# Performance work log

Hardware: AMD Instinct MI355X
Metric: run time of the kernel (lower is better)

## Reference

```python
import jax, jax.numpy as jnp
import numpy as np

N_NODES = 200000
N_EDGES = 800000
N_GRAPHS = 4096
ATOM_DIM = 128
HIDDEN = 256
LN_EPS = 1e-5


def _layer_norm(x, g, b):
    m = jnp.mean(x, axis=-1, keepdims=True)
    v = jnp.mean((x - m) ** 2, axis=-1, keepdims=True)
    return (x - m) / jnp.sqrt(v + LN_EPS) * g + b


def setup_inputs() -> dict:
    key = jax.random.key(0)
    ks = jax.random.split(key, 16)
    d = {}
    d['x'] = jax.random.normal(ks[0], (N_NODES, ATOM_DIM), dtype=jnp.float32)
    d['edge_index'] = jax.random.randint(ks[1], (2, N_EDGES), 0, N_NODES, dtype=jnp.int32)
    # sorted batch assignment covering all graphs (PyG batches are sorted)
    d['batch'] = ((jnp.arange(N_NODES) * N_GRAPHS) // N_NODES).astype(jnp.int32)

    def glorot(k, shape):
        fan_in, fan_out = shape[0], shape[1]
        s = jnp.sqrt(2.0 / (fan_in + fan_out))
        return jax.random.normal(k, shape, dtype=jnp.float32) * s

    d['gin1_w1'] = glorot(ks[2], (ATOM_DIM, HIDDEN)); d['gin1_b1'] = jnp.zeros((HIDDEN,), jnp.float32)
    d['gin1_w2'] = glorot(ks[3], (HIDDEN, HIDDEN));  d['gin1_b2'] = jnp.zeros((HIDDEN,), jnp.float32)
    d['gin2_w1'] = glorot(ks[4], (HIDDEN, HIDDEN));  d['gin2_b1'] = jnp.zeros((HIDDEN,), jnp.float32)
    d['gin2_w2'] = glorot(ks[5], (HIDDEN, HIDDEN));  d['gin2_b2'] = jnp.zeros((HIDDEN,), jnp.float32)
    d['ln_g'] = jnp.ones((HIDDEN,), jnp.float32);    d['ln_b'] = jnp.zeros((HIDDEN,), jnp.float32)
    d['s2_w1'] = glorot(ks[6], (HIDDEN, 768));       d['s2_b1'] = jnp.zeros((768,), jnp.float32)
    d['s2_ln_g'] = jnp.ones((768,), jnp.float32);    d['s2_ln_b'] = jnp.zeros((768,), jnp.float32)
    d['s2_w2'] = glorot(ks[7], (768, 2));            d['s2_b2'] = jnp.zeros((2,), jnp.float32)
    return d


def reference(x, edge_index, batch,
              gin1_w1, gin1_b1, gin1_w2, gin1_b2,
              gin2_w1, gin2_b1, gin2_w2, gin2_b2,
              ln_g, ln_b,
              s2_w1, s2_b1, s2_ln_g, s2_ln_b, s2_w2, s2_b2):
    src, dst = edge_index[0], edge_index[1]

    def gin_conv(h, w1, b1, w2, b2):
        # GINConv: mlp((1+eps)*x + sum_{j in N(i)} x_j), eps=0
        agg = jax.ops.segment_sum(h[src], dst, num_segments=h.shape[0])
        z = h + agg
        return jax.nn.relu(z @ w1 + b1) @ w2 + b2

    h = gin_conv(x, gin1_w1, gin1_b1, gin1_w2, gin1_b2)
    h = jax.nn.leaky_relu(_layer_norm(h, ln_g, ln_b), 0.2)
    h = gin_conv(h, gin2_w1, gin2_b1, gin2_w2, gin2_b2)
    h = jax.nn.leaky_relu(h, 0.2)
    # global max pool over graphs
    g = jax.ops.segment_max(h, batch, num_segments=N_GRAPHS)
    # seq2 head (dropout = identity in eval)
    z = jax.nn.leaky_relu(_layer_norm(g @ s2_w1 + s2_b1, s2_ln_g, s2_ln_b), 0.2)
    z = z @ s2_w2 + s2_b2
    return jax.nn.softmax(z, axis=-1)
```

## Files before the change

### kernel.cpp

```cpp
#include <hip/hip_runtime.h>

#define NN 200000
#define NE 800000
#define NG 4096
#define AD 128
#define HD 256
#define LN_EPS 1e-5f
#define NB 782

typedef __attribute__((ext_vector_type(8))) short     bf16x8;
typedef __attribute__((ext_vector_type(8))) unsigned short us8;
typedef __attribute__((ext_vector_type(4))) float     f32x4;

__device__ __forceinline__ float leaky(float v){ return v > 0.f ? v : 0.2f*v; }

__device__ __forceinline__ unsigned short f2bf(float f){
  unsigned u = __float_as_uint(f);
  return (unsigned short)((u + 0x7FFFu + ((u >> 16) & 1u)) >> 16);
}
__device__ __forceinline__ float bf2f(unsigned short h){ return __uint_as_float(((unsigned)h) << 16); }

__device__ __forceinline__ unsigned fkey(float f){
  unsigned u = __float_as_uint(f);
  return (u & 0x80000000u) ? ~u : (u | 0x80000000u);
}
__device__ __forceinline__ float fdec(unsigned k){
  return (k & 0x80000000u) ? __uint_as_float(k & 0x7FFFFFFFu) : __uint_as_float(~k);
}

__global__ __launch_bounds__(256) void k_zero(int* __restrict__ cur){
  int i = blockIdx.x * 256 + threadIdx.x;
  if (i < NN) cur[i] = 0;
}

__global__ __launch_bounds__(256) void k_count(const int* __restrict__ ei, int* __restrict__ cur){
  int e = blockIdx.x * 256 + threadIdx.x;
  atomicAdd(&cur[ei[NE + e]], 1);
}

__global__ __launch_bounds__(256) void k_scanA(const int* __restrict__ cur, int* __restrict__ partial){
  __shared__ int sd[256];
  int t = threadIdx.x, b = blockIdx.x, i = b * 256 + t;
  sd[t] = (i < NN) ? cur[i] : 0;
  __syncthreads();
  for (int off = 128; off >= 1; off >>= 1){
    if (t < off) sd[t] += sd[t + off];
    __syncthreads();
  }
  if (t == 0) partial[b] = sd[0];
}

__global__ __launch_bounds__(1024) void k_scanB(const int* __restrict__ partial,
                                                int* __restrict__ scanoff, int* __restrict__ rowptr){
  __shared__ int sd[1024];
  int t = threadIdx.x;
  int v = (t < NB) ? partial[t] : 0;
  sd[t] = v; __syncthreads();
  for (int off = 1; off < 1024; off <<= 1){
    int u = (t >= off) ? sd[t - off] : 0;
    __syncthreads();
    sd[t] += u;
    __syncthreads();
  }
  if (t < NB) scanoff[t] = sd[t] - v;
  if (t == 0) rowptr[NN] = NE;
}

__global__ __launch_bounds__(256) void k_scanC(int* __restrict__ cur, const int* __restrict__ scanoff,
                                               int* __restrict__ rowptr){
  __shared__ int sd[256];
  int t = threadIdx.x, b = blockIdx.x, i = b * 256 + t;
  int v = (i < NN) ? cur[i] : 0;
  sd[t] = v; __syncthreads();
  for (int off = 1; off < 256; off <<= 1){
    int u = (t >= off) ? sd[t - off] : 0;
    __syncthreads();
    sd[t] += u;
    __syncthreads();
  }
  if (i < NN){ rowptr[i] = scanoff[b] + sd[t] - v; cur[i] = 0; }
}

__global__ __launch_bounds__(256) void k_fill(const int* __restrict__ ei,
                                              const int* __restrict__ rowptr,
                                              int* __restrict__ cur,
                                              int* __restrict__ col){
  int e = blockIdx.x * 256 + threadIdx.x;
  int s = ei[e], d = ei[NE + e];
  int pos = atomicAdd(&cur[d], 1);
  col[rowptr[d] + pos] = s;
}

__global__ __launch_bounds__(256) void k_initG(unsigned* __restrict__ Gk){
  int i = blockIdx.x * 256 + threadIdx.x;
  Gk[i] = 0x00800000u;
}

__global__ __launch_bounds__(256) void k_wprep(const float* __restrict__ src,
                                               unsigned short* __restrict__ dst, int K){
  int k = blockIdx.x, n = threadIdx.x;
  dst[(size_t)n * K + k] = f2bf(src[(size_t)k * 256 + n]);
}

__global__ __launch_bounds__(256) void k_layer1(const float* __restrict__ x,
                                                const int* __restrict__ rowptr,
                                                const int* __restrict__ col,
                                                const unsigned short* __restrict__ W1T,
                                                const float* __restrict__ b1,
                                                const unsigned short* __restrict__ W2T,
                                                const float* __restrict__ b2,
                                                const float* __restrict__ lng,
                                                const float* __restrict__ lnb,
                                                unsigned short* __restrict__ H1){
  __shared__ alignas(16) char sS[16 * 256 + 16 * 512];
  __shared__ float2 redS[16][4];
  char* zS = sS;
  char* tS = sS + 4096;
  const int tid = threadIdx.x;
  const int l = tid & 63, wv = tid >> 6;
  const int cl = l & 15, kg = l >> 4;
  const int row0 = blockIdx.x * 16;

  {
    const int row = tid >> 4, sub = tid & 15;
    const int grow = row0 + row;
    const float4* x4 = (const float4*)x;
    float4 s0 = x4[(size_t)grow * 32 + sub * 2];
    float4 s1 = x4[(size_t)grow * 32 + sub * 2 + 1];
    float a[8] = {s0.x, s0.y, s0.z, s0.w, s1.x, s1.y, s1.z, s1.w};
    const int p = rowptr[grow], pe = rowptr[grow + 1];
    int q = p;
    for (; q + 4 <= pe; q += 4){
      int j0 = col[q], j1 = col[q+1], j2 = col[q+2], j3 = col[q+3];
      float4 b00 = x4[(size_t)j0*32 + sub*2], b01 = x4[(size_t)j0*32 + sub*2 + 1];
      float4 b10 = x4[(size_t)j1*32 + sub*2], b11 = x4[(size_t)j1*32 + sub*2 + 1];
      float4 b20 = x4[(size_t)j2*32 + sub*2], b21 = x4[(size_t)j2*32 + sub*2 + 1];
      float4 b30 = x4[(size_t)j3*32 + sub*2], b31 = x4[(size_t)j3*32 + sub*2 + 1];
      a[0] += (b00.x + b10.x) + (b20.x + b30.x);
      a[1] += (b00.y + b10.y) + (b20.y + b30.y);
      a[2] += (b00.z + b10.z) + (b20.z + b30.z);
      a[3] += (b00.w + b10.w) + (b20.w + b30.w);
      a[4] += (b01.x + b11.x) + (b21.x + b31.x);
      a[5] += (b01.y + b11.y) + (b21.y + b31.y);
      a[6] += (b01.z + b11.z) + (b21.z + b31.z);
      a[7] += (b01.w + b11.w) + (b21.w + b31.w);
    }
    for (; q < pe; ++q){
      int j = col[q];
      float4 c0 = x4[(size_t)j*32 + sub*2], c1 = x4[(size_t)j*32 + sub*2 + 1];
      a[0]+=c0.x; a[1]+=c0.y; a[2]+=c0.z; a[3]+=c0.w;
      a[4]+=c1.x; a[5]+=c1.y; a[6]+=c1.z; a[7]+=c1.w;
    }
    us8 o;
    #pragma unroll
    for (int j = 0; j < 8; ++j) o[j] = f2bf(a[j]);
    *(us8*)&zS[row * 256 + ((sub * 16) ^ ((row & 7) << 4))] = o;
  }
  __syncthreads();

  f32x4 acc[4];
  #pragma unroll
  for (int nt = 0; nt < 4; ++nt){
    float bv = b1[wv * 64 + nt * 16 + cl];
    acc[nt] = (f32x4){bv, bv, bv, bv};
  }
  #pragma unroll
  for (int ks = 0; ks < 4; ++ks){
    const int kb = (ks * 32 + kg * 8) * 2;
    bf16x8 a0 = *(const bf16x8*)&zS[cl * 256 + (kb ^ ((cl & 7) << 4))];
    #pragma unroll
    for (int nt = 0; nt < 4; ++nt){
      bf16x8 b = *(const bf16x8*)(W1T + (size_t)(wv * 64 + nt * 16 + cl) * AD + ks * 32 + kg * 8);
      acc[nt] = __builtin_amdgcn_mfma_f32_16x16x32_bf16(a0, b, acc[nt], 0, 0, 0);
    }
  }
  #pragma unroll
  for (int nt = 0; nt < 4; ++nt)
    #pragma unroll
    for (int rg = 0; rg < 4; ++rg){
      float v = fmaxf(acc[nt][rg], 0.f);
      int row = kg * 4 + rg;
      int cc = wv * 64 + nt * 16 + cl;
      *(unsigned short*)&tS[row * 512 + ((cc * 2) ^ ((row & 7) << 4))] = f2bf(v);
    }
  __syncthreads();

  #pragma unroll
  for (int nt = 0; nt < 4; ++nt){
    float bv = b2[wv * 64 + nt * 16 + cl];
    acc[nt] = (f32x4){bv, bv, bv, bv};
  }
  #pragma unroll
  for (int ks = 0; ks < 8; ++ks){
    const int kb = (ks * 32 + kg * 8) * 2;
    bf16x8 a0 = *(const bf16x8*)&tS[cl * 512 + (kb ^ ((cl & 7) << 4))];
    #pragma unroll
    for (int nt = 0; nt < 4; ++nt){
      bf16x8 b = *(const bf16x8*)(W2T + (size_t)(wv * 64 + nt * 16 + cl) * HD + ks * 32 + kg * 8);
      acc[nt] = __builtin_amdgcn_mfma_f32_16x16x32_bf16(a0, b, acc[nt], 0, 0, 0);
    }
  }

  float s1v[4], s2v[4];
  #pragma unroll
  for (int rg = 0; rg < 4; ++rg){
    float a = acc[0][rg] + acc[1][rg] + acc[2][rg] + acc[3][rg];
    float b = acc[0][rg]*acc[0][rg] + acc[1][rg]*acc[1][rg]
            + acc[2][rg]*acc[2][rg] + acc[3][rg]*acc[3][rg];
    #pragma unroll
    for (int off = 1; off <= 8; off <<= 1){ a += __shfl_xor(a, off); b += __shfl_xor(b, off); }
    s1v[rg] = a; s2v[rg] = b;
  }
  if (cl == 0){
    #pragma unroll
    for (int rg = 0; rg < 4; ++rg)
      redS[kg * 4 + rg][wv] = make_float2(s1v[rg], s2v[rg]);
  }
  __syncthreads();
  #pragma unroll
  for (int rg = 0; rg < 4; ++rg){
    int row = kg * 4 + rg;
    float t1 = redS[row][0].x + redS[row][1].x + redS[row][2].x + redS[row][3].x;
    float t2 = redS[row][0].y + redS[row][1].y + redS[row][2].y + redS[row][3].y;
    float m  = t1 * (1.f / HD);
    float vr = t2 * (1.f / HD) - m * m;
    float rs = rsqrtf(vr + LN_EPS);
    #pragma unroll
    for (int nt = 0; nt < 4; ++nt){
      int cc = wv * 64 + nt * 16 + cl;
      float v = (acc[nt][rg] - m) * rs * lng[cc] + lnb[cc];
      H1[(size_t)(row0 + row) * HD + cc] = f2bf(leaky(v));
    }
  }
}

__global__ __launch_bounds__(256) void k_layer2(const unsigned short* __restrict__ H1,
                                                const int* __restrict__ rowptr,
                                                const int* __restrict__ col,
                                                const int* __restrict__ batch,
                                                const unsigned short* __restrict__ W1T,
                                                const float* __restrict__ b1,
                                                const unsigned short* __restrict__ W2T,
                                                const float* __restrict__ b2,
                                                unsigned* __restrict__ Gk){
  __shared__ alignas(16) char sS[16 * 512 * 2];
  char* zS = sS;
  char* tS = sS + 8192;
  float* stageF = (float*)sS;
  const int tid = threadIdx.x;
  const int l = tid & 63, wv = tid >> 6;
  const int cl = l & 15, kg = l >> 4;
  const int row0 = blockIdx.x * 16;

  {
    const int row = tid >> 4, sub = tid & 15;
    const int grow = row0 + row;
    us8 a0 = *(const us8*)(H1 + (size_t)grow * HD + sub * 16);
    us8 a1 = *(const us8*)(H1 + (size_t)grow * HD + sub * 16 + 8);
    float a[16];
    #pragma unroll
    for (int j = 0; j < 8; ++j){ a[j] = bf2f(a0[j]); a[8 + j] = bf2f(a1[j]); }
    const int p = rowptr[grow], pe = rowptr[grow + 1];
    int q = p;
    for (; q + 4 <= pe; q += 4){
      int j0 = col[q], j1 = col[q+1], j2 = col[q+2], j3 = col[q+3];
      us8 b00 = *(const us8*)(H1 + (size_t)j0*HD + sub*16), b01 = *(const us8*)(H1 + (size_t)j0*HD + sub*16 + 8);
      us8 b10 = *(const us8*)(H1 + (size_t)j1*HD + sub*16), b11 = *(const us8*)(H1 + (size_t)j1*HD + sub*16 + 8);
      us8 b20 = *(const us8*)(H1 + (size_t)j2*HD + sub*16), b21 = *(const us8*)(H1 + (size_t)j2*HD + sub*16 + 8);
      us8 b30 = *(const us8*)(H1 + (size_t)j3*HD + sub*16), b31 = *(const us8*)(H1 + (size_t)j3*HD + sub*16 + 8);
      #pragma unroll
      for (int j = 0; j < 8; ++j){
        a[j]     += (bf2f(b00[j]) + bf2f(b10[j])) + (bf2f(b20[j]) + bf2f(b30[j]));
        a[8 + j] += (bf2f(b01[j]) + bf2f(b11[j])) + (bf2f(b21[j]) + bf2f(b31[j]));
      }
    }
    for (; q < pe; ++q){
      int jn = col[q];
      us8 c0 = *(const us8*)(H1 + (size_t)jn*HD + sub*16), c1 = *(const us8*)(H1 + (size_t)jn*HD + sub*16 + 8);
      #pragma unroll
      for (int j = 0; j < 8; ++j){ a[j] += bf2f(c0[j]); a[8 + j] += bf2f(c1[j]); }
    }
    us8 o0, o1;
    #pragma unroll
    for (int j = 0; j < 8; ++j){ o0[j] = f2bf(a[j]); o1[j] = f2bf(a[8 + j]); }
    const int swz = (row & 7) << 4;
    *(us8*)&zS[row * 512 + ((sub * 32) ^ swz)]      = o0;
    *(us8*)&zS[row * 512 + ((sub * 32 + 16) ^ swz)] = o1;
  }
  __syncthreads();

  f32x4 acc[4];
  #pragma unroll
  for (int nt = 0; nt < 4; ++nt){
    float bv = b1[wv * 64 + nt * 16 + cl];
    acc[nt] = (f32x4){bv, bv, bv, bv};
  }
  #pragma unroll
  for (int ks = 0; ks < 8; ++ks){
    const int kb = (ks * 32 + kg * 8) * 2;
    bf16x8 a0 = *(const bf16x8*)&zS[cl * 512 + (kb ^ ((cl & 7) << 4))];
    #pragma unroll
    for (int nt = 0; nt < 4; ++nt){
      bf16x8 b = *(const bf16x8*)(W1T + (size_t)(wv * 64 + nt * 16 + cl) * HD + ks * 32 + kg * 8);
      acc[nt] = __builtin_amdgcn_mfma_f32_16x16x32_bf16(a0, b, acc[nt], 0, 0, 0);
    }
  }
  #pragma unroll
  for (int nt = 0; nt < 4; ++nt)
    #pragma unroll
    for (int rg = 0; rg < 4; ++rg){
      float v = fmaxf(acc[nt][rg], 0.f);
      int row = kg * 4 + rg;
      int cc = wv * 64 + nt * 16 + cl;
      *(unsigned short*)&tS[row * 512 + ((cc * 2) ^ ((row & 7) << 4))] = f2bf(v);
    }
  __syncthreads();

  #pragma unroll
  for (int nt = 0; nt < 4; ++nt){
    float bv = b2[wv * 64 + nt * 16 + cl];
    acc[nt] = (f32x4){bv, bv, bv, bv};
  }
  #pragma unroll
  for (int ks = 0; ks < 8; ++ks){
    const int kb = (ks * 32 + kg * 8) * 2;
    bf16x8 a0 = *(const bf16x8*)&tS[cl * 512 + (kb ^ ((cl & 7) << 4))];
    #pragma unroll
    for (int nt = 0; nt < 4; ++nt){
      bf16x8 b = *(const bf16x8*)(W2T + (size_t)(wv * 64 + nt * 16 + cl) * HD + ks * 32 + kg * 8);
      acc[nt] = __builtin_amdgcn_mfma_f32_16x16x32_bf16(a0, b, acc[nt], 0, 0, 0);
    }
  }
  __syncthreads();

  #pragma unroll
  for (int nt = 0; nt < 4; ++nt)
    #pragma unroll
    for (int rg = 0; rg < 4; ++rg){
      int row = kg * 4 + rg;
      int cc = wv * 64 + nt * 16 + cl;
      stageF[row * HD + cc] = leaky(acc[nt][rg]);
    }
  __syncthreads();

  {
    const int c = tid;
    int gprev = batch[row0];
    float m = -3.4e38f;
    #pragma unroll
    for (int r = 0; r < 16; ++r){
      int g = batch[row0 + r];
      if (g != gprev){
        atomicMax(&Gk[(size_t)gprev * HD + c], fkey(m));
        m = -3.4e38f;
        gprev = g;
      }
      m = fmaxf(m, stageF[r * HD + c]);
    }
    atomicMax(&Gk[(size_t)gprev * HD + c], fkey(m));
  }
}

__global__ __launch_bounds__(256) void head_kernel(const unsigned* __restrict__ Gk,
                                                   const float* __restrict__ w1,
                                                   const float* __restrict__ b1,
                                                   const float* __restrict__ lng,
                                                   const float* __restrict__ lnb,
                                                   const float* __restrict__ w2,
                                                   const float* __restrict__ b2,
                                                   float* __restrict__ out){
  __shared__ float gs[8][256];
  __shared__ float redA[8][4], redB[8][4];
  const int tid = threadIdx.x;
  const int g0 = blockIdx.x * 8;
  #pragma unroll
  for (int q = 0; q < 8; ++q) gs[q][tid] = fdec(Gk[(size_t)(g0 + q) * 256 + tid]);
  __syncthreads();

  float z[8][3];
  #pragma unroll
  for (int j = 0; j < 3; ++j){
    const int c = tid + j * 256;
    float a[8];
    float bv = b1[c];
    #pragma unroll
    for (int q = 0; q < 8; ++q) a[q] = bv;
    #pragma unroll 8
    for (int k = 0; k < 256; ++k){
      float w = w1[(size_t)k * 768 + c];
      #pragma unroll
      for (int q = 0; q < 8; ++q) a[q] += gs[q][k] * w;
    }
    #pragma unroll
    for (int q = 0; q < 8; ++q) z[q][j] = a[q];
  }

  const int lane = tid & 63, wv = tid >> 6;
  float mean[8], rs[8];
  {
    float s1[8], s2[8];
    #pragma unroll
    for (int q = 0; q < 8; ++q){
      s1[q] = z[q][0] + z[q][1] + z[q][2];
      s2[q] = z[q][0]*z[q][0] + z[q][1]*z[q][1] + z[q][2]*z[q][2];
    }
    #pragma unroll
    for (int off = 32; off >= 1; off >>= 1){
      #pragma unroll
      for (int q = 0; q < 8; ++q){ s1[q] += __shfl_xor(s1[q], off); s2[q] += __shfl_xor(s2[q], off); }
    }
    if (lane == 0){
      #pragma unroll
      for (int q = 0; q < 8; ++q){ redA[q][wv] = s1[q]; redB[q][wv] = s2[q]; }
    }
    __syncthreads();
    #pragma unroll
    for (int q = 0; q < 8; ++q){
      float t1 = redA[q][0] + redA[q][1] + redA[q][2] + redA[q][3];
      float t2 = redB[q][0] + redB[q][1] + redB[q][2] + redB[q][3];
      float m = t1 * (1.f / 768.f);
      float v = t2 * (1.f / 768.f) - m * m;
      mean[q] = m; rs[q] = rsqrtf(v + LN_EPS);
    }
  }
  __syncthreads();

  float p0[8], p1[8];
  #pragma unroll
  for (int q = 0; q < 8; ++q){ p0[q] = 0.f; p1[q] = 0.f; }
  #pragma unroll
  for (int j = 0; j < 3; ++j){
    const int c = tid + j * 256;
    float gcol = lng[c], bcol = lnb[c];
    float wa = w2[2 * c], wb = w2[2 * c + 1];
    #pragma unroll
    for (int q = 0; q < 8; ++q){
      float zz = leaky((z[q][j] - mean[q]) * rs[q] * gcol + bcol);
      p0[q] += zz * wa; p1[q] += zz * wb;
    }
  }
  #pragma unroll
  for (int off = 32; off >= 1; off >>= 1){
    #pragma unroll
    for (int q = 0; q < 8; ++q){ p0[q] += __shfl_xor(p0[q], off); p1[q] += __shfl_xor(p1[q], off); }
  }
  if (lane == 0){
    #pragma unroll
    for (int q = 0; q < 8; ++q){ redA[q][wv] = p0[q]; redB[q][wv] = p1[q]; }
  }
  __syncthreads();
  if (tid < 8){
    int q = tid;
    float l0 = redA[q][0] + redA[q][1] + redA[q][2] + redA[q][3] + b2[0];
    float l1 = redB[q][0] + redB[q][1] + redB[q][2] + redB[q][3] + b2[1];
    float mm = fmaxf(l0, l1);
    float e0 = expf(l0 - mm), e1 = expf(l1 - mm);
    float inv = 1.f / (e0 + e1);
    out[(size_t)(g0 + q) * 2 + 0] = e0 * inv;
    out[(size_t)(g0 + q) * 2 + 1] = e1 * inv;
  }
}

extern "C" void kernel_launch(void* const* d_in, const int* in_sizes, int n_in,
                              void* d_out, int out_size, void* d_ws, size_t ws_size,
                              hipStream_t stream){
  const float* x     = (const float*)d_in[0];
  const int*   ei    = (const int*)  d_in[1];
  const int*   batch = (const int*)  d_in[2];
  const float* g1w1  = (const float*)d_in[3];
  const float* g1b1  = (const float*)d_in[4];
  const float* g1w2  = (const float*)d_in[5];
  const float* g1b2  = (const float*)d_in[6];
  const float* g2w1  = (const float*)d_in[7];
  const float* g2b1  = (const float*)d_in[8];
  const float* g2w2  = (const float*)d_in[9];
  const float* g2b2  = (const float*)d_in[10];
  const float* lng   = (const float*)d_in[11];
  const float* lnb   = (const float*)d_in[12];
  const float* s2w1  = (const float*)d_in[13];
  const float* s2b1  = (const float*)d_in[14];
  const float* s2lng = (const float*)d_in[15];
  const float* s2lnb = (const float*)d_in[16];
  const float* s2w2  = (const float*)d_in[17];
  const float* s2b2  = (const float*)d_in[18];
  float* out = (float*)d_out;

  char* ws = (char*)d_ws;
  int*            rowptr  = (int*)(ws + 0);
  int*            col     = (int*)(ws + 800032);
  unsigned*       Gk      = (unsigned*)(ws + 4000032);
  int*            cur     = (int*)Gk;
  unsigned short* W1T1    = (unsigned short*)(ws + 8194336);
  unsigned short* W2T1    = (unsigned short*)(ws + 8259872);
  unsigned short* W1T2    = (unsigned short*)(ws + 8390944);
  unsigned short* W2T2    = (unsigned short*)(ws + 8522016);
  int*            partial = (int*)(ws + 8653088);
  int*            scanoff = (int*)(ws + 8657184);
  unsigned short* H1      = (unsigned short*)(ws + 8661280);

  k_zero <<<(NN + 255) / 256, 256, 0, stream>>>(cur);
  k_count<<<NE / 256,         256, 0, stream>>>(ei, cur);
  k_scanA<<<NB,               256, 0, stream>>>(cur, partial);
  k_scanB<<<1,               1024, 0, stream>>>(partial, scanoff, rowptr);
  k_scanC<<<NB,               256, 0, stream>>>(cur, scanoff, rowptr);
  k_fill <<<NE / 256,         256, 0, stream>>>(ei, rowptr, cur, col);
  k_initG<<<NG * HD / 256,    256, 0, stream>>>(Gk);
  k_wprep<<<128, 256, 0, stream>>>(g1w1, W1T1, 128);
  k_wprep<<<256, 256, 0, stream>>>(g1w2, W2T1, 256);
  k_wprep<<<256, 256, 0, stream>>>(g2w1, W1T2, 256);
  k_wprep<<<256, 256, 0, stream>>>(g2w2, W2T2, 256);
  k_layer1<<<NN / 16, 256, 0, stream>>>(x, rowptr, col, W1T1, g1b1, W2T1, g1b2, lng, lnb, H1);
  k_layer2<<<NN / 16, 256, 0, stream>>>(H1, rowptr, col, batch, W1T2, g2b1, W2T2, g2b2, Gk);
  head_kernel<<<NG / 8, 256, 0, stream>>>(Gk, s2w1, s2b1, s2lng, s2lnb, s2w2, s2b2, out);
}
```

Before: 916.4 us.

## Gather neighbor rows with one wavefront per row and shuffled column indices

Restructures the neighbor-aggregation phase in both GIN layer kernels so that each wavefront handles one node row at a time (four passes over 16 rows). The row's column indices are loaded cooperatively and broadcast with shuffles. This replaces the old scheme where 16 threads covered a row and each thread looped over that row's neighbor list on its own. The aim is to balance degree variance across lanes and make each gather fully coalesced, at the cost of serialising four rows per wave and using narrower per-lane loads.

```diff
diff --git a/kernel.cpp b/kernel.cpp
--- a/kernel.cpp
+++ b/kernel.cpp
@@ -10,6 +10,7 @@
 
 typedef __attribute__((ext_vector_type(8))) short     bf16x8;
 typedef __attribute__((ext_vector_type(8))) unsigned short us8;
+typedef __attribute__((ext_vector_type(4))) unsigned short us4;
 typedef __attribute__((ext_vector_type(4))) float     f32x4;
 
 __device__ __forceinline__ float leaky(float v){ return v > 0.f ? v : 0.2f*v; }
@@ -121,40 +122,34 @@
   const int cl = l & 15, kg = l >> 4;
   const int row0 = blockIdx.x * 16;
 
-  {
-    const int row = tid >> 4, sub = tid & 15;
-    const int grow = row0 + row;
-    const float4* x4 = (const float4*)x;
-    float4 s0 = x4[(size_t)grow * 32 + sub * 2];
-    float4 s1 = x4[(size_t)grow * 32 + sub * 2 + 1];
-    float a[8] = {s0.x, s0.y, s0.z, s0.w, s1.x, s1.y, s1.z, s1.w};
-    const int p = rowptr[grow], pe = rowptr[grow + 1];
-    int q = p;
-    for (; q + 4 <= pe; q += 4){
-      int j0 = col[q], j1 = col[q+1], j2 = col[q+2], j3 = col[q+3];
-      float4 b00 = x4[(size_t)j0*32 + sub*2], b01 = x4[(size_t)j0*32 + sub*2 + 1];
-      float4 b10 = x4[(size_t)j1*32 + sub*2], b11 = x4[(size_t)j1*32 + sub*2 + 1];
-      float4 b20 = x4[(size_t)j2*32 + sub*2], b21 = x4[(size_t)j2*32 + sub*2 + 1];
-      float4 b30 = x4[(size_t)j3*32 + sub*2], b31 = x4[(size_t)j3*32 + sub*2 + 1];
-      a[0] += (b00.x + b10.x) + (b20.x + b30.x);
-      a[1] += (b00.y + b10.y) + (b20.y + b30.y);
-      a[2] += (b00.z + b10.z) + (b20.z + b30.z);
-      a[3] += (b00.w + b10.w) + (b20.w + b30.w);
-      a[4] += (b01.x + b11.x) + (b21.x + b31.x);
-      a[5] += (b01.y + b11.y) + (b21.y + b31.y);
-      a[6] += (b01.z + b11.z) + (b21.z + b31.z);
-      a[7] += (b01.w + b11.w) + (b21.w + b31.w);
-    }
-    for (; q < pe; ++q){
-      int j = col[q];
-      float4 c0 = x4[(size_t)j*32 + sub*2], c1 = x4[(size_t)j*32 + sub*2 + 1];
-      a[0]+=c0.x; a[1]+=c0.y; a[2]+=c0.z; a[3]+=c0.w;
-      a[4]+=c1.x; a[5]+=c1.y; a[6]+=c1.z; a[7]+=c1.w;
-    }
-    us8 o;
-    #pragma unroll
-    for (int j = 0; j < 8; ++j) o[j] = f2bf(a[j]);
-    *(us8*)&zS[row * 256 + ((sub * 16) ^ ((row & 7) << 4))] = o;
+  const float2* x2 = (const float2*)x;
+  #pragma unroll
+  for (int pass = 0; pass < 4; ++pass){
+    const int r = pass * 4 + wv;
+    const int row = row0 + r;
+    float2 s = x2[(size_t)row * 64 + l];
+    float ax = s.x, ay = s.y;
+    const int p = rowptr[row], pe = rowptr[row + 1];
+    for (int base = p; base < pe; base += 64){
+      const int nn = min(64, pe - base);
+      int idx = col[base + (l < nn ? l : 0)];
+      int q = 0;
+      for (; q + 4 <= nn; q += 4){
+        int j0 = __shfl(idx, q),     j1 = __shfl(idx, q + 1);
+        int j2 = __shfl(idx, q + 2), j3 = __shfl(idx, q + 3);
+        float2 b0 = x2[(size_t)j0 * 64 + l], b1v = x2[(size_t)j1 * 64 + l];
+        float2 b2v = x2[(size_t)j2 * 64 + l], b3 = x2[(size_t)j3 * 64 + l];
+        ax += (b0.x + b1v.x) + (b2v.x + b3.x);
+        ay += (b0.y + b1v.y) + (b2v.y + b3.y);
+      }
+      for (; q < nn; ++q){
+        int j = __shfl(idx, q);
+        float2 b = x2[(size_t)j * 64 + l];
+        ax += b.x; ay += b.y;
+      }
+    }
+    unsigned pk = (unsigned)f2bf(ax) | ((unsigned)f2bf(ay) << 16);
+    *(unsigned*)&zS[r * 256 + ((l * 4) ^ ((r & 7) << 4))] = pk;
   }
   __syncthreads();
 
@@ -252,40 +247,37 @@
   const int cl = l & 15, kg = l >> 4;
   const int row0 = blockIdx.x * 16;
 
-  {
-    const int row = tid >> 4, sub = tid & 15;
-    const int grow = row0 + row;
-    us8 a0 = *(const us8*)(H1 + (size_t)grow * HD + sub * 16);
-    us8 a1 = *(const us8*)(H1 + (size_t)grow * HD + sub * 16 + 8);
-    float a[16];
-    #pragma unroll
-    for (int j = 0; j < 8; ++j){ a[j] = bf2f(a0[j]); a[8 + j] = bf2f(a1[j]); }
-    const int p = rowptr[grow], pe = rowptr[grow + 1];
-    int q = p;
-    for (; q + 4 <= pe; q += 4){
-      int j0 = col[q], j1 = col[q+1], j2 = col[q+2], j3 = col[q+3];
-      us8 b00 = *(const us8*)(H1 + (size_t)j0*HD + sub*16), b01 = *(const us8*)(H1 + (size_t)j0*HD + sub*16 + 8);
-      us8 b10 = *(const us8*)(H1 + (size_t)j1*HD + sub*16), b11 = *(const us8*)(H1 + (size_t)j1*HD + sub*16 + 8);
-      us8 b20 = *(const us8*)(H1 + (size_t)j2*HD + sub*16), b21 = *(const us8*)(H1 + (size_t)j2*HD + sub*16 + 8);
-      us8 b30 = *(const us8*)(H1 + (size_t)j3*HD + sub*16), b31 = *(const us8*)(H1 + (size_t)j3*HD + sub*16 + 8);
-      #pragma unroll
-      for (int j = 0; j < 8; ++j){
-        a[j]     += (bf2f(b00[j]) + bf2f(b10[j])) + (bf2f(b20[j]) + bf2f(b30[j]));
-        a[8 + j] += (bf2f(b01[j]) + bf2f(b11[j])) + (bf2f(b21[j]) + bf2f(b31[j]));
+  #pragma unroll
+  for (int pass = 0; pass < 4; ++pass){
+    const int r = pass * 4 + wv;
+    const int row = row0 + r;
+    us4 s = *(const us4*)(H1 + (size_t)row * HD + l * 4);
+    float f0 = bf2f(s[0]), f1 = bf2f(s[1]), f2 = bf2f(s[2]), f3 = bf2f(s[3]);
+    const int p = rowptr[row], pe = rowptr[row + 1];
+    for (int base = p; base < pe; base += 64){
+      const int nn = min(64, pe - base);
+      int idx = col[base + (l < nn ? l : 0)];
+      int q = 0;
+      for (; q + 4 <= nn; q += 4){
+        int j0 = __shfl(idx, q),     j1 = __shfl(idx, q + 1);
+        int j2 = __shfl(idx, q + 2), j3 = __shfl(idx, q + 3);
+        us4 b0 = *(const us4*)(H1 + (size_t)j0 * HD + l * 4);
+        us4 b1v = *(const us4*)(H1 + (size_t)j1 * HD + l * 4);
+        us4 b2v = *(const us4*)(H1 + (size_t)j2 * HD + l * 4);
+        us4 b3 = *(const us4*)(H1 + (size_t)j3 * HD + l * 4);
+        f0 += (bf2f(b0[0]) + bf2f(b1v[0])) + (bf2f(b2v[0]) + bf2f(b3[0]));
+        f1 += (bf2f(b0[1]) + bf2f(b1v[1])) + (bf2f(b2v[1]) + bf2f(b3[1]));
+        f2 += (bf2f(b0[2]) + bf2f(b1v[2])) + (bf2f(b2v[2]) + bf2f(b3[2]));
+        f3 += (bf2f(b0[3]) + bf2f(b1v[3])) + (bf2f(b2v[3]) + bf2f(b3[3]));
       }
-    }
-    for (; q < pe; ++q){
-      int jn = col[q];
-      us8 c0 = *(const us8*)(H1 + (size_t)jn*HD + sub*16), c1 = *(const us8*)(H1 + (size_t)jn*HD + sub*16 + 8);
-      #pragma unroll
-      for (int j = 0; j < 8; ++j){ a[j] += bf2f(c0[j]); a[8 + j] += bf2f(c1[j]); }
-    }
-    us8 o0, o1;
-    #pragma unroll
-    for (int j = 0; j < 8; ++j){ o0[j] = f2bf(a[j]); o1[j] = f2bf(a[8 + j]); }
-    const int swz = (row & 7) << 4;
-    *(us8*)&zS[row * 512 + ((sub * 32) ^ swz)]      = o0;
-    *(us8*)&zS[row * 512 + ((sub * 32 + 16) ^ swz)] = o1;
+      for (; q < nn; ++q){
+        int j = __shfl(idx, q);
+        us4 b = *(const us4*)(H1 + (size_t)j * HD + l * 4);
+        f0 += bf2f(b[0]); f1 += bf2f(b[1]); f2 += bf2f(b[2]); f3 += bf2f(b[3]);
+      }
+    }
+    us4 o; o[0] = f2bf(f0); o[1] = f2bf(f1); o[2] = f2bf(f2); o[3] = f2bf(f3);
+    *(us4*)&zS[r * 512 + ((l * 8) ^ ((r & 7) << 4))] = o;
   }
   __syncthreads();
 
```

Result: slower. 963.6 us (+5.2%).

## Stage neighbor rows into LDS via global_load_lds in GIN aggregation

Applied to the files above, without the earlier changes.

Replaces per-thread gathered global loads of neighbor feature rows with a block-cooperative scheme. Each 64-edge chunk of the block's CSR range is fetched directly into shared memory with global_load_lds, then each thread sums its node's rows from LDS. The aim is fully coalesced 512-byte row transfers and better memory-level parallelism for the random gather. The cost is a much larger LDS footprint, which lowers occupancy, plus two barriers per chunk.

```diff
diff --git a/kernel.cpp b/kernel.cpp
--- a/kernel.cpp
+++ b/kernel.cpp
@@ -10,7 +10,11 @@
 
 typedef __attribute__((ext_vector_type(8))) short     bf16x8;
 typedef __attribute__((ext_vector_type(8))) unsigned short us8;
+typedef __attribute__((ext_vector_type(4))) unsigned short us4;
 typedef __attribute__((ext_vector_type(4))) float     f32x4;
+
+typedef __attribute__((address_space(1))) const unsigned gl_t;
+typedef __attribute__((address_space(3))) unsigned       ld_t;
 
 __device__ __forceinline__ float leaky(float v){ return v > 0.f ? v : 0.2f*v; }
 
@@ -112,49 +116,61 @@
                                                 const float* __restrict__ lng,
                                                 const float* __restrict__ lnb,
                                                 unsigned short* __restrict__ H1){
-  __shared__ alignas(16) char sS[16 * 256 + 16 * 512];
+  __shared__ alignas(16) char gbuf[32768 + 4096];
   __shared__ float2 redS[16][4];
-  char* zS = sS;
-  char* tS = sS + 4096;
+  char* zS = gbuf + 32768;
+  char* tS = gbuf;
   const int tid = threadIdx.x;
   const int l = tid & 63, wv = tid >> 6;
   const int cl = l & 15, kg = l >> 4;
   const int row0 = blockIdx.x * 16;
-
+  const int r16 = tid >> 4, sub = tid & 15;
+  const int grow = row0 + r16;
+
+  const float4* x4 = (const float4*)x;
+  float a[8];
   {
-    const int row = tid >> 4, sub = tid & 15;
-    const int grow = row0 + row;
-    const float4* x4 = (const float4*)x;
     float4 s0 = x4[(size_t)grow * 32 + sub * 2];
     float4 s1 = x4[(size_t)grow * 32 + sub * 2 + 1];
-    float a[8] = {s0.x, s0.y, s0.z, s0.w, s1.x, s1.y, s1.z, s1.w};
-    const int p = rowptr[grow], pe = rowptr[grow + 1];
-    int q = p;
-    for (; q + 4 <= pe; q += 4){
-      int j0 = col[q], j1 = col[q+1], j2 = col[q+2], j3 = col[q+3];
-      float4 b00 = x4[(size_t)j0*32 + sub*2], b01 = x4[(size_t)j0*32 + sub*2 + 1];
-      float4 b10 = x4[(size_t)j1*32 + sub*2], b11 = x4[(size_t)j1*32 + sub*2 + 1];
-      float4 b20 = x4[(size_t)j2*32 + sub*2], b21 = x4[(size_t)j2*32 + sub*2 + 1];
-      float4 b30 = x4[(size_t)j3*32 + sub*2], b31 = x4[(size_t)j3*32 + sub*2 + 1];
-      a[0] += (b00.x + b10.x) + (b20.x + b30.x);
-      a[1] += (b00.y + b10.y) + (b20.y + b30.y);
-      a[2] += (b00.z + b10.z) + (b20.z + b30.z);
-      a[3] += (b00.w + b10.w) + (b20.w + b30.w);
-      a[4] += (b01.x + b11.x) + (b21.x + b31.x);
-      a[5] += (b01.y + b11.y) + (b21.y + b31.y);
-      a[6] += (b01.z + b11.z) + (b21.z + b31.z);
-      a[7] += (b01.w + b11.w) + (b21.w + b31.w);
-    }
-    for (; q < pe; ++q){
-      int j = col[q];
-      float4 c0 = x4[(size_t)j*32 + sub*2], c1 = x4[(size_t)j*32 + sub*2 + 1];
-      a[0]+=c0.x; a[1]+=c0.y; a[2]+=c0.z; a[3]+=c0.w;
-      a[4]+=c1.x; a[5]+=c1.y; a[6]+=c1.z; a[7]+=c1.w;
-    }
+    a[0]=s0.x; a[1]=s0.y; a[2]=s0.z; a[3]=s0.w; a[4]=s1.x; a[5]=s1.y; a[6]=s1.z; a[7]=s1.w;
+  }
+  const int pr = rowptr[grow], per = rowptr[grow + 1];
+  const int p0 = rowptr[row0], pend = rowptr[row0 + 16];
+
+  for (int cs = p0; cs < pend; cs += 64){
+    const int ns = min(64, pend - cs);
+    {
+      const int cidx = cs + wv * 16 + (l & 15);
+      int colv = (cidx < pend) ? col[cidx] : 0;
+      #pragma unroll
+      for (int i = 0; i < 8; ++i){
+        const int lslot = wv * 16 + i * 2 + (l >> 5);
+        const int j = __shfl(colv, i * 2 + (l >> 5));
+        if (lslot < ns){
+          const void* src = (const void*)(x + (size_t)j * AD + (l & 31) * 4);
+          void* dst = (void*)(gbuf + (wv * 16 + i * 2) * 512);
+          __builtin_amdgcn_global_load_lds((gl_t*)src, (ld_t*)dst, 16, 0, 0);
+        }
+      }
+    }
+    __syncthreads();
+    {
+      const int qlo = max(pr, cs), qhi = min(per, cs + ns);
+      for (int q = qlo; q < qhi; ++q){
+        const float4* lrow = (const float4*)(gbuf + (q - cs) * 512 + sub * 32);
+        float4 c0 = lrow[0], c1 = lrow[1];
+        a[0]+=c0.x; a[1]+=c0.y; a[2]+=c0.z; a[3]+=c0.w;
+        a[4]+=c1.x; a[5]+=c1.y; a[6]+=c1.z; a[7]+=c1.w;
+      }
+    }
+    __syncthreads();
+  }
+
+  {
     us8 o;
     #pragma unroll
     for (int j = 0; j < 8; ++j) o[j] = f2bf(a[j]);
-    *(us8*)&zS[row * 256 + ((sub * 16) ^ ((row & 7) << 4))] = o;
+    *(us8*)&zS[r16 * 256 + ((sub * 16) ^ ((r16 & 7) << 4))] = o;
   }
   __syncthreads();
 
@@ -204,12 +220,12 @@
   float s1v[4], s2v[4];
   #pragma unroll
   for (int rg = 0; rg < 4; ++rg){
-    float a = acc[0][rg] + acc[1][rg] + acc[2][rg] + acc[3][rg];
-    float b = acc[0][rg]*acc[0][rg] + acc[1][rg]*acc[1][rg]
-            + acc[2][rg]*acc[2][rg] + acc[3][rg]*acc[3][rg];
-    #pragma unroll
-    for (int off = 1; off <= 8; off <<= 1){ a += __shfl_xor(a, off); b += __shfl_xor(b, off); }
-    s1v[rg] = a; s2v[rg] = b;
+    float aa = acc[0][rg] + acc[1][rg] + acc[2][rg] + acc[3][rg];
+    float bb = acc[0][rg]*acc[0][rg] + acc[1][rg]*acc[1][rg]
+             + acc[2][rg]*acc[2][rg] + acc[3][rg]*acc[3][rg];
+    #pragma unroll
+    for (int off = 1; off <= 8; off <<= 1){ aa += __shfl_xor(aa, off); bb += __shfl_xor(bb, off); }
+    s1v[rg] = aa; s2v[rg] = bb;
   }
   if (cl == 0){
     #pragma unroll
@@ -243,49 +259,63 @@
                                                 const unsigned short* __restrict__ W2T,
                                                 const float* __restrict__ b2,
                                                 unsigned* __restrict__ Gk){
-  __shared__ alignas(16) char sS[16 * 512 * 2];
-  char* zS = sS;
-  char* tS = sS + 8192;
-  float* stageF = (float*)sS;
+  __shared__ alignas(16) char gbuf[32768 + 8192];
+  char* zS = gbuf + 32768;
+  char* tS = gbuf;
+  float* stageF = (float*)gbuf;
   const int tid = threadIdx.x;
   const int l = tid & 63, wv = tid >> 6;
   const int cl = l & 15, kg = l >> 4;
   const int row0 = blockIdx.x * 16;
-
+  const int r16 = tid >> 4, sub = tid & 15;
+  const int grow = row0 + r16;
+
+  float a[16];
   {
-    const int row = tid >> 4, sub = tid & 15;
-    const int grow = row0 + row;
     us8 a0 = *(const us8*)(H1 + (size_t)grow * HD + sub * 16);
     us8 a1 = *(const us8*)(H1 + (size_t)grow * HD + sub * 16 + 8);
-    float a[16];
     #pragma unroll
     for (int j = 0; j < 8; ++j){ a[j] = bf2f(a0[j]); a[8 + j] = bf2f(a1[j]); }
-    const int p = rowptr[grow], pe = rowptr[grow + 1];
-    int q = p;
-    for (; q + 4 <= pe; q += 4){
-      int j0 = col[q], j1 = col[q+1], j2 = col[q+2], j3 = col[q+3];
-      us8 b00 = *(const us8*)(H1 + (size_t)j0*HD + sub*16), b01 = *(const us8*)(H1 + (size_t)j0*HD + sub*16 + 8);
-      us8 b10 = *(const us8*)(H1 + (size_t)j1*HD + sub*16), b11 = *(const us8*)(H1 + (size_t)j1*HD + sub*16 + 8);
-      us8 b20 = *(const us8*)(H1 + (size_t)j2*HD + sub*16), b21 = *(const us8*)(H1 + (size_t)j2*HD + sub*16 + 8);
-      us8 b30 = *(const us8*)(H1 + (size_t)j3*HD + sub*16), b31 = *(const us8*)(H1 + (size_t)j3*HD + sub*16 + 8);
+  }
+  const int pr = rowptr[grow], per = rowptr[grow + 1];
+  const int p0 = rowptr[row0], pend = rowptr[row0 + 16];
+
+  for (int cs = p0; cs < pend; cs += 64){
+    const int ns = min(64, pend - cs);
+    {
+      const int cidx = cs + wv * 16 + (l & 15);
+      int colv = (cidx < pend) ? col[cidx] : 0;
       #pragma unroll
-      for (int j = 0; j < 8; ++j){
-        a[j]     += (bf2f(b00[j]) + bf2f(b10[j])) + (bf2f(b20[j]) + bf2f(b30[j]));
-        a[8 + j] += (bf2f(b01[j]) + bf2f(b11[j])) + (bf2f(b21[j]) + bf2f(b31[j]));
+      for (int i = 0; i < 8; ++i){
+        const int lslot = wv * 16 + i * 2 + (l >> 5);
+        const int j = __shfl(colv, i * 2 + (l >> 5));
+        if (lslot < ns){
+          const void* src = (const void*)(H1 + (size_t)j * HD + (l & 31) * 8);
+          void* dst = (void*)(gbuf + (wv * 16 + i * 2) * 512);
+          __builtin_amdgcn_global_load_lds((gl_t*)src, (ld_t*)dst, 16, 0, 0);
+        }
       }
     }
-    for (; q < pe; ++q){
-      int jn = col[q];
-      us8 c0 = *(const us8*)(H1 + (size_t)jn*HD + sub*16), c1 = *(const us8*)(H1 + (size_t)jn*HD + sub*16 + 8);
-      #pragma unroll
-      for (int j = 0; j < 8; ++j){ a[j] += bf2f(c0[j]); a[8 + j] += bf2f(c1[j]); }
-    }
+    __syncthreads();
+    {
+      const int qlo = max(pr, cs), qhi = min(per, cs + ns);
+      for (int q = qlo; q < qhi; ++q){
+        const us8* lrow = (const us8*)(gbuf + (q - cs) * 512 + sub * 32);
+        us8 c0 = lrow[0], c1 = lrow[1];
+        #pragma unroll
+        for (int j = 0; j < 8; ++j){ a[j] += bf2f(c0[j]); a[8 + j] += bf2f(c1[j]); }
+      }
+    }
+    __syncthreads();
+  }
+
+  {
     us8 o0, o1;
     #pragma unroll
     for (int j = 0; j < 8; ++j){ o0[j] = f2bf(a[j]); o1[j] = f2bf(a[8 + j]); }
-    const int swz = (row & 7) << 4;
-    *(us8*)&zS[row * 512 + ((sub * 32) ^ swz)]      = o0;
-    *(us8*)&zS[row * 512 + ((sub * 32 + 16) ^ swz)] = o1;
+    const int swz = (r16 & 7) << 4;
+    *(us8*)&zS[r16 * 512 + ((sub * 32) ^ swz)]      = o0;
+    *(us8*)&zS[r16 * 512 + ((sub * 32 + 16) ^ swz)] = o1;
   }
   __syncthreads();
 
```

Result: no change. 899.5 us (median of 2 runs) (-1.8%).
